# Performance work log

Measured on AMD Instinct MI355X. Metric: run time of the kernel, lower is better.

Reference implementation:

```python
import jax, jax.numpy as jnp
import numpy as np

B, T, H, F, K, NB, MAXL = 32, 512, 512, 512, 3, 256, 2048


def _conv1d(x, w, b, pad):
    # x: [B,T,Cin], w: [K,Cin,Cout] -> [B,T,Cout]
    y = jax.lax.conv_general_dilated(x, w, window_strides=(1,), padding=[(pad, pad)],
                                     dimension_numbers=('NWC', 'WIO', 'NWC'))
    return y + b


def _layernorm(x, g, b):
    m = jnp.mean(x, axis=-1, keepdims=True)
    v = jnp.mean((x - m) ** 2, axis=-1, keepdims=True)
    return (x - m) * jax.lax.rsqrt(v + 1e-5) * g + b


def _variance_predictor(x, mask, cw1, cb1, g1, b1, cw2, cb2, g2, b2, lw, lb, k):
    # ConvNorm(k, pad=(k-1)//2) -> ReLU -> LN -> ConvNorm(k, pad=1) -> ReLU -> LN -> Linear(F,1)
    h = _layernorm(jax.nn.relu(_conv1d(x, cw1, cb1, (k - 1) // 2)), g1, b1)
    h = _layernorm(jax.nn.relu(_conv1d(h, cw2, cb2, 1)), g2, b2)
    out = h @ lw + lb  # [B,T]
    return jnp.where(mask, 0.0, out)


def setup_inputs() -> dict:
    key = jax.random.key(0)
    ks = jax.random.split(key, 12)
    s = 0.02
    inp = {
        'x': jax.random.normal(ks[0], (B, T, H), jnp.float32),
        'src_mask': jnp.zeros((B, T), jnp.bool_),
        'duration': jax.random.randint(ks[1], (B, T), 0, 8),
        'pitch_target': jax.random.normal(ks[2], (B, T), jnp.float32),
        'energy_target': jax.random.normal(ks[3], (B, T), jnp.float32),
        # stacked predictor params: index 0=duration, 1=pitch, 2=energy
        'conv1_w': jax.random.normal(ks[4], (3, K, H, F), jnp.float32) * s,
        'conv1_b': jnp.zeros((3, F), jnp.float32),
        'ln1_g': jnp.ones((3, F), jnp.float32),
        'ln1_b': jnp.zeros((3, F), jnp.float32),
        'conv2_w': jax.random.normal(ks[5], (3, K, F, F), jnp.float32) * s,
        'conv2_b': jnp.zeros((3, F), jnp.float32),
        'ln2_g': jnp.ones((3, F), jnp.float32),
        'ln2_b': jnp.zeros((3, F), jnp.float32),
        'lin_w': jax.random.normal(ks[6], (3, F), jnp.float32) * s,
        'lin_b': jnp.zeros((3,), jnp.float32),
        'pitch_bins': jnp.linspace(-3.0, 3.0, NB - 1, dtype=jnp.float32),
        'energy_bins': jnp.linspace(-3.0, 3.0, NB - 1, dtype=jnp.float32),
        'pitch_table': jax.random.normal(ks[7], (NB, H), jnp.float32) * s,
        'energy_table': jax.random.normal(ks[8], (NB, H), jnp.float32) * s,
        'max_len': MAXL,
    }
    return inp


def reference(x, src_mask, duration, pitch_target, energy_target,
              conv1_w, conv1_b, ln1_g, ln1_b, conv2_w, conv2_b, ln2_g, ln2_b,
              lin_w, lin_b, pitch_bins, energy_bins, pitch_table, energy_table, max_len):
    k = conv1_w.shape[1]

    def vp(i, inp):
        return _variance_predictor(inp, src_mask, conv1_w[i], conv1_b[i], ln1_g[i], ln1_b[i],
                                   conv2_w[i], conv2_b[i], ln2_g[i], ln2_b[i], lin_w[i], lin_b[i], k)

    log_duration_pred = vp(0, x)
    # pitch: predict, bucketize target, add embedding (training path with targets)
    pitch_pred = vp(1, x)
    p_idx = jnp.searchsorted(pitch_bins, pitch_target)  # torch.bucketize
    x = x + pitch_table[p_idx]
    # energy on pitch-conditioned features
    energy_pred = vp(2, x)
    e_idx = jnp.searchsorted(energy_bins, energy_target)
    x = x + energy_table[e_idx]

    # LengthRegulator: expand each phoneme vec duration[b,i] times, pad to max_len
    dur = jnp.where(src_mask, 0, duration)
    cum = jnp.cumsum(dur, axis=1)                 # [B,T]
    mel_len = jnp.minimum(cum[:, -1], max_len)    # [B]
    frames = jnp.arange(max_len)
    idx = jax.vmap(lambda c: jnp.searchsorted(c, frames, side='right'))(cum)
    idx = jnp.clip(idx, 0, x.shape[1] - 1)        # [B,max_len]
    x_out = jnp.take_along_axis(x, idx[:, :, None], axis=1)  # [B,max_len,H]
    mel_mask = frames[None, :] >= mel_len[:, None]
    x_out = jnp.where(mel_mask[:, :, None], 0.0, x_out)
    return x_out, log_duration_pred, pitch_pred, energy_pred, mel_len, mel_mask
```

## Files before the change

### kernel.cpp

```cpp
#include <hip/hip_runtime.h>
#include <hip/hip_bf16.h>

typedef unsigned short ushort_t;
typedef unsigned int uint_t;
typedef __attribute__((ext_vector_type(8))) short bf16x8;
typedef __attribute__((ext_vector_type(4))) float f32x4;

#define NB_T 512
#define NB_B 32
#define NB_M (NB_B * NB_T)
#define KDIM 1536
#define MAXL 2048
#define EPI_STRIDE 144

__device__ __forceinline__ ushort_t f2bf(float f) {
  __hip_bfloat16 h = __float2bfloat16(f);
  return *reinterpret_cast<ushort_t*>(&h);
}
__device__ __forceinline__ float bf2f(ushort_t u) {
  __hip_bfloat16 h;
  *reinterpret_cast<ushort_t*>(&h) = u;
  return __bfloat162float(h);
}
__device__ __forceinline__ uint_t pack2(float a, float b) {
  return (uint_t)f2bf(a) | ((uint_t)f2bf(b) << 16);
}
__device__ __forceinline__ void gload_lds16(const void* g, void* l) {
  __builtin_amdgcn_global_load_lds((const __attribute__((address_space(1))) void*)g,
                                   (__attribute__((address_space(3))) void*)l, 16, 0, 0);
}

__global__ __launch_bounds__(256) void k_wt(const float* __restrict__ w, ushort_t* __restrict__ wt) {
  __shared__ float tile[64][65];
  const int pk = blockIdx.y;
  const int p = pk / 3, kk = pk % 3;
  const int ot = (blockIdx.x & 7) * 64;
  const int it = (blockIdx.x >> 3) * 64;
  const int tx = threadIdx.x & 63;
  const int ty = threadIdx.x >> 6;
  const float* src = w + (size_t)pk * 512 * 512;
  #pragma unroll
  for (int r = ty; r < 64; r += 4)
    tile[r][tx] = src[(size_t)(it + r) * 512 + ot + tx];
  __syncthreads();
  #pragma unroll
  for (int r = ty; r < 64; r += 4)
    wt[((size_t)(p * 512 + ot + r)) * KDIM + kk * 512 + it + tx] = f2bf(tile[tx][r]);
}

__global__ __launch_bounds__(256) void k_bucket(const float* __restrict__ pt, const float* __restrict__ et,
                                                const float* __restrict__ pb, const float* __restrict__ eb,
                                                int* __restrict__ pi, int* __restrict__ ei) {
  const int i = blockIdx.x * 256 + threadIdx.x;
  if (i >= NB_M) return;
  float v = pt[i];
  int lo = 0, hi = 255;
  while (lo < hi) { int mid = (lo + hi) >> 1; if (pb[mid] < v) lo = mid + 1; else hi = mid; }
  pi[i] = lo;
  v = et[i]; lo = 0; hi = 255;
  while (lo < hi) { int mid = (lo + hi) >> 1; if (eb[mid] < v) lo = mid + 1; else hi = mid; }
  ei[i] = lo;
}

__global__ __launch_bounds__(512) void k_cum(const int* __restrict__ dur, const unsigned char* __restrict__ mask,
                                             int* __restrict__ cum, float* __restrict__ mel_len_out,
                                             float* __restrict__ mel_mask_out) {
  __shared__ int s[512];
  const int b = blockIdx.x, t = threadIdx.x;
  int d = mask[b * NB_T + t] ? 0 : dur[b * NB_T + t];
  s[t] = d;
  __syncthreads();
  for (int off = 1; off < 512; off <<= 1) {
    int v = (t >= off) ? s[t - off] : 0;
    __syncthreads();
    s[t] += v;
    __syncthreads();
  }
  cum[b * NB_T + t] = s[t];
  int ml = s[511]; ml = ml < MAXL ? ml : MAXL;
  if (t == 0) mel_len_out[b] = (float)ml;
  for (int f = t; f < MAXL; f += 512)
    mel_mask_out[b * MAXL + f] = (f >= ml) ? 1.0f : 0.0f;
}

__global__ __launch_bounds__(256) void k_prep(const float* __restrict__ x,
                                              const float* __restrict__ ptab, const float* __restrict__ etab,
                                              const int* __restrict__ pidx, const int* __restrict__ eidx,
                                              ushort_t* __restrict__ xb_pad, ushort_t* __restrict__ x2pad,
                                              ushort_t* __restrict__ lnp2, float* __restrict__ x3f) {
  const int rp = blockIdx.x;
  const int b = rp / 514, j = rp % 514;
  const int tid = threadIdx.x;
  if (j == 0 || j == 513) {
    ((uint_t*)(xb_pad + (size_t)rp * 512))[tid] = 0u;
    ((uint_t*)(x2pad + (size_t)rp * 512))[tid] = 0u;
    ((uint_t*)(lnp2 + (size_t)rp * 512))[tid] = 0u;
    return;
  }
  const int m = b * NB_T + j - 1;
  const float2 xv = ((const float2*)(x + (size_t)m * 512))[tid];
  const float2 pv = ((const float2*)(ptab + (size_t)pidx[m] * 512))[tid];
  const float2 ev = ((const float2*)(etab + (size_t)eidx[m] * 512))[tid];
  ((uint_t*)(xb_pad + (size_t)rp * 512))[tid] = pack2(xv.x, xv.y);
  const float ax = xv.x + pv.x, ay = xv.y + pv.y;
  ((uint_t*)(x2pad + (size_t)rp * 512))[tid] = pack2(ax, ay);
  float2 o; o.x = ax + ev.x; o.y = ay + ev.y;
  ((float2*)(x3f + (size_t)m * 512))[tid] = o;
}

__global__ __launch_bounds__(256) void k_gemm(const ushort_t* __restrict__ A0,
                                              const ushort_t* __restrict__ A1,
                                              const ushort_t* __restrict__ A2,
                                              const ushort_t* __restrict__ Wt,
                                              const float* __restrict__ bias,
                                              ushort_t* __restrict__ H) {
  __shared__ short smem[18432];
  const int tid = threadIdx.x;
  const int lane = tid & 63, wid = tid >> 6;

  const int h = blockIdx.x;
  const int logical = (h & 7) * 192 + (h >> 3);
  const int pred = logical >> 9;
  const int tile = logical & 511;
  const int mt = tile >> 2, nt = tile & 3;
  const int m0 = mt * 128, n0 = nt * 128;
  const int b = m0 >> 9, t0 = m0 & 511;
  const long Arow0 = (long)b * 514 + t0 + 1;

  const ushort_t* Ap = (pred == 0) ? A0 : ((pred == 1) ? A1 : A2);
  const ushort_t* Wp = Wt + (size_t)pred * 512 * KDIM;
  const float* bp = bias + pred * 512;
  ushort_t* Hp = H + (size_t)pred * NB_M * 512;

  const int subr = lane >> 2;
  const int ioff = (lane & 3) * 8;
  const int wr = wid >> 1, wc = wid & 1;
  const int lr = lane & 15, kg = lane >> 4;

  f32x4 acc[4][4];
  #pragma unroll
  for (int i = 0; i < 4; ++i)
    #pragma unroll
    for (int j = 0; j < 4; ++j) acc[i][j] = (f32x4)0.f;

  auto STAGE = [&](int kk, int buf) {
    const int dt = (kk >> 4) - 1;
    const int i0 = (kk & 15) << 5;
    short* la = &smem[buf * 8192];
    short* lb = &smem[buf * 8192 + 4096];
    #pragma unroll
    for (int q = 0; q < 2; ++q) {
      const int chunk = wid * 2 + q;
      const int r = chunk * 16 + subr;
      gload_lds16(Ap + (size_t)(Arow0 + r + dt) * 512 + i0 + ioff, &la[chunk * 512]);
      gload_lds16(Wp + (size_t)(n0 + r) * KDIM + kk * 32 + ioff, &lb[chunk * 512]);
    }
  };

  STAGE(0, 0);
  __syncthreads();
  int buf = 0;
  for (int kk = 0; kk < 48; ++kk) {
    if (kk < 47) STAGE(kk + 1, buf ^ 1);
    const short* la = &smem[buf * 8192];
    const short* lb = &smem[buf * 8192 + 4096];
    bf16x8 af[4], bfv[4];
    #pragma unroll
    for (int fi = 0; fi < 4; ++fi)
      af[fi] = *(const bf16x8*)&la[(wr * 64 + fi * 16 + lr) * 32 + kg * 8];
    #pragma unroll
    for (int fj = 0; fj < 4; ++fj)
      bfv[fj] = *(const bf16x8*)&lb[(wc * 64 + fj * 16 + lr) * 32 + kg * 8];
    #pragma unroll
    for (int fi = 0; fi < 4; ++fi)
      #pragma unroll
      for (int fj = 0; fj < 4; ++fj)
        acc[fi][fj] = __builtin_amdgcn_mfma_f32_16x16x32_bf16(af[fi], bfv[fj], acc[fi][fj], 0, 0, 0);
    __syncthreads();
    buf ^= 1;
  }

  float bvv[4];
  #pragma unroll
  for (int fj = 0; fj < 4; ++fj) bvv[fj] = bp[n0 + wc * 64 + fj * 16 + lr];
  #pragma unroll
  for (int fi = 0; fi < 4; ++fi) {
    const int rowb = wr * 64 + fi * 16 + kg * 4;
    #pragma unroll
    for (int fj = 0; fj < 4; ++fj) {
      const int col = wc * 64 + fj * 16 + lr;
      #pragma unroll
      for (int r = 0; r < 4; ++r) {
        float v = acc[fi][fj][r] + bvv[fj];
        v = v > 0.f ? v : 0.f;
        smem[(rowb + r) * EPI_STRIDE + col] = (short)f2bf(v);
      }
    }
  }
  __syncthreads();
  #pragma unroll
  for (int s = 0; s < 8; ++s) {
    const int chunk = tid + s * 256;
    const int row = chunk >> 4, c8 = (chunk & 15) * 8;
    bf16x8 vv = *(const bf16x8*)&smem[row * EPI_STRIDE + c8];
    *(bf16x8*)(Hp + (size_t)(m0 + row) * 512 + n0 + c8) = vv;
  }
}

__global__ __launch_bounds__(256) void k_ln_mid(const ushort_t* __restrict__ Hh,
                                                const float* __restrict__ g, const float* __restrict__ bb,
                                                ushort_t* __restrict__ lnp0, ushort_t* __restrict__ lnp1,
                                                ushort_t* __restrict__ lnp2) {
  const int rr = blockIdx.x * 4 + (threadIdx.x >> 6);
  const int pred = rr >> 14, m = rr & (NB_M - 1);
  const int lane = threadIdx.x & 63;
  const float* gp = g + pred * 512;
  const float* bp = bb + pred * 512;
  ushort_t* dst = (pred == 0) ? lnp0 : ((pred == 1) ? lnp1 : lnp2);
  bf16x8 v = *(const bf16x8*)(Hh + (size_t)rr * 512 + lane * 8);
  float xv[8];
  float s = 0.f;
  #pragma unroll
  for (int j = 0; j < 8; ++j) { xv[j] = bf2f((ushort_t)v[j]); s += xv[j]; }
  #pragma unroll
  for (int mm = 32; mm >= 1; mm >>= 1) s += __shfl_xor(s, mm, 64);
  const float mean = s * (1.f / 512.f);
  float vs = 0.f;
  #pragma unroll
  for (int j = 0; j < 8; ++j) { float d = xv[j] - mean; vs += d * d; }
  #pragma unroll
  for (int mm = 32; mm >= 1; mm >>= 1) vs += __shfl_xor(vs, mm, 64);
  const float rstd = rsqrtf(vs * (1.f / 512.f) + 1e-5f);
  const float4 g0 = ((const float4*)(gp + lane * 8))[0];
  const float4 g1 = ((const float4*)(gp + lane * 8))[1];
  const float4 b0 = ((const float4*)(bp + lane * 8))[0];
  const float4 b1 = ((const float4*)(bp + lane * 8))[1];
  const float gg[8] = {g0.x, g0.y, g0.z, g0.w, g1.x, g1.y, g1.z, g1.w};
  const float bv[8] = {b0.x, b0.y, b0.z, b0.w, b1.x, b1.y, b1.z, b1.w};
  bf16x8 o;
  #pragma unroll
  for (int j = 0; j < 8; ++j) o[j] = (short)f2bf((xv[j] - mean) * rstd * gg[j] + bv[j]);
  const int bidx = m >> 9, t = m & 511;
  *(bf16x8*)(dst + ((size_t)(bidx * 514 + t + 1)) * 512 + lane * 8) = o;
}

__global__ __launch_bounds__(256) void k_ln_fin(const ushort_t* __restrict__ Hh,
                                                const float* __restrict__ g, const float* __restrict__ bb,
                                                const float* __restrict__ lw, const float* __restrict__ lbp,
                                                const unsigned char* __restrict__ mask,
                                                float* __restrict__ outp) {
  const int rr = blockIdx.x * 4 + (threadIdx.x >> 6);
  const int pred = rr >> 14, m = rr & (NB_M - 1);
  const int lane = threadIdx.x & 63;
  const float* gp = g + pred * 512;
  const float* bp = bb + pred * 512;
  const float* wp = lw + pred * 512;
  bf16x8 v = *(const bf16x8*)(Hh + (size_t)rr * 512 + lane * 8);
  float xv[8];
  float s = 0.f;
  #pragma unroll
  for (int j = 0; j < 8; ++j) { xv[j] = bf2f((ushort_t)v[j]); s += xv[j]; }
  #pragma unroll
  for (int mm = 32; mm >= 1; mm >>= 1) s += __shfl_xor(s, mm, 64);
  const float mean = s * (1.f / 512.f);
  float vs = 0.f;
  #pragma unroll
  for (int j = 0; j < 8; ++j) { float d = xv[j] - mean; vs += d * d; }
  #pragma unroll
  for (int mm = 32; mm >= 1; mm >>= 1) vs += __shfl_xor(vs, mm, 64);
  const float rstd = rsqrtf(vs * (1.f / 512.f) + 1e-5f);
  const float4 g0 = ((const float4*)(gp + lane * 8))[0];
  const float4 g1 = ((const float4*)(gp + lane * 8))[1];
  const float4 b0 = ((const float4*)(bp + lane * 8))[0];
  const float4 b1 = ((const float4*)(bp + lane * 8))[1];
  const float4 w0 = ((const float4*)(wp + lane * 8))[0];
  const float4 w1 = ((const float4*)(wp + lane * 8))[1];
  const float gg[8] = {g0.x, g0.y, g0.z, g0.w, g1.x, g1.y, g1.z, g1.w};
  const float bv[8] = {b0.x, b0.y, b0.z, b0.w, b1.x, b1.y, b1.z, b1.w};
  const float ww[8] = {w0.x, w0.y, w0.z, w0.w, w1.x, w1.y, w1.z, w1.w};
  float dot = 0.f;
  #pragma unroll
  for (int j = 0; j < 8; ++j) dot += ((xv[j] - mean) * rstd * gg[j] + bv[j]) * ww[j];
  #pragma unroll
  for (int mm = 32; mm >= 1; mm >>= 1) dot += __shfl_xor(dot, mm, 64);
  if (lane == 0) {
    float val = dot + lbp[pred];
    if (mask[m]) val = 0.f;
    outp[pred * NB_M + m] = val;
  }
}

__global__ __launch_bounds__(128) void k_regulate(const float* __restrict__ x3f, const int* __restrict__ cum,
                                                  float* __restrict__ xout) {
  const int bid = blockIdx.x;
  const int b = bid >> 11, f = bid & 2047;
  const int* c = cum + b * NB_T;
  int ml = c[511]; ml = ml < MAXL ? ml : MAXL;
  const int tid = threadIdx.x;
  float4 val = make_float4(0.f, 0.f, 0.f, 0.f);
  if (f < ml) {
    int lo = 0, hi = 512;
    while (lo < hi) { int mid = (lo + hi) >> 1; if (c[mid] <= f) lo = mid + 1; else hi = mid; }
    if (lo > 511) lo = 511;
    val = ((const float4*)(x3f + ((size_t)(b * NB_T + lo)) * 512))[tid];
  }
  ((float4*)(xout + ((size_t)(b * MAXL + f)) * 512))[tid] = val;
}

extern "C" void kernel_launch(void* const* d_in, const int* in_sizes, int n_in,
                              void* d_out, int out_size, void* d_ws, size_t ws_size,
                              hipStream_t stream) {
  const float* x        = (const float*)d_in[0];
  const unsigned char* src_mask = (const unsigned char*)d_in[1];
  const int* duration   = (const int*)d_in[2];
  const float* pitch_t  = (const float*)d_in[3];
  const float* energy_t = (const float*)d_in[4];
  const float* conv1_w  = (const float*)d_in[5];
  const float* conv1_b  = (const float*)d_in[6];
  const float* ln1_g    = (const float*)d_in[7];
  const float* ln1_b    = (const float*)d_in[8];
  const float* conv2_w  = (const float*)d_in[9];
  const float* conv2_b  = (const float*)d_in[10];
  const float* ln2_g    = (const float*)d_in[11];
  const float* ln2_b    = (const float*)d_in[12];
  const float* lin_w    = (const float*)d_in[13];
  const float* lin_b    = (const float*)d_in[14];
  const float* pbins    = (const float*)d_in[15];
  const float* ebins    = (const float*)d_in[16];
  const float* ptab     = (const float*)d_in[17];
  const float* etab     = (const float*)d_in[18];

  char* ws = (char*)d_ws;
  ushort_t* wt1    = (ushort_t*)(ws + 0);
  ushort_t* wt2    = (ushort_t*)(ws + 4718592);
  ushort_t* xb_pad = (ushort_t*)(ws + 9437184);
  ushort_t* x2pad  = (ushort_t*)(ws + 26279936);
  ushort_t* lnp2   = (ushort_t*)(ws + 43122688);
  ushort_t* hbuf   = (ushort_t*)(ws + 59965440);
  float*    x3f    = (float*)   (ws + 110297088);
  int*      p_idx  = (int*)     (ws + 143851520);
  int*      e_idx  = (int*)     (ws + 143917056);
  int*      cum    = (int*)     (ws + 143982592);

  float* out      = (float*)d_out;
  float* o_xout   = out;
  float* o_preds  = out + 33554432;
  float* o_mellen = o_preds + 3 * NB_M;
  float* o_mmask  = o_mellen + 32;

  k_bucket<<<NB_M / 256, 256, 0, stream>>>(pitch_t, energy_t, pbins, ebins, p_idx, e_idx);
  k_cum<<<NB_B, 512, 0, stream>>>(duration, src_mask, cum, o_mellen, o_mmask);
  k_wt<<<dim3(64, 9), 256, 0, stream>>>(conv1_w, wt1);
  k_wt<<<dim3(64, 9), 256, 0, stream>>>(conv2_w, wt2);
  k_prep<<<NB_B * 514, 256, 0, stream>>>(x, ptab, etab, p_idx, e_idx, xb_pad, x2pad, lnp2, x3f);

  k_gemm<<<1536, 256, 0, stream>>>(xb_pad, xb_pad, x2pad, wt1, conv1_b, hbuf);
  k_ln_mid<<<3 * NB_M / 4, 256, 0, stream>>>(hbuf, ln1_g, ln1_b, xb_pad, x2pad, lnp2);
  k_gemm<<<1536, 256, 0, stream>>>(xb_pad, x2pad, lnp2, wt2, conv2_b, hbuf);
  k_ln_fin<<<3 * NB_M / 4, 256, 0, stream>>>(hbuf, ln2_g, ln2_b, lin_w, lin_b, src_mask, o_preds);

  k_regulate<<<NB_B * MAXL, 128, 0, stream>>>(x3f, cum, o_xout);
}
```

Before: 503.2 us.

## Fuse bucketize into prep, merge weight transposes, store x3 in bf16, restructure regulate

The bucketize binary search moves into k_prep, which removes a kernel launch and the p_idx/e_idx round trip. The two weight-transpose launches become a single launch. The pitch- and energy-conditioned features are stored as bf16 instead of fp32, halving that intermediate write and the regulator's gather reads. k_regulate is rewritten so each block caches the cumsum in LDS, handles 64 frames and also writes mel_mask, which lets k_cum drop that write; the cost is bf16 rounding on the x_out output values.

```diff
diff --git a/kernel.cpp b/kernel.cpp
--- a/kernel.cpp
+++ b/kernel.cpp
@@ -30,41 +30,30 @@
                                    (__attribute__((address_space(3))) void*)l, 16, 0, 0);
 }
 
-__global__ __launch_bounds__(256) void k_wt(const float* __restrict__ w, ushort_t* __restrict__ wt) {
+__global__ __launch_bounds__(256) void k_wt(const float* __restrict__ w1, const float* __restrict__ w2,
+                                            ushort_t* __restrict__ wt1, ushort_t* __restrict__ wt2) {
   __shared__ float tile[64][65];
-  const int pk = blockIdx.y;
-  const int p = pk / 3, kk = pk % 3;
+  int g = blockIdx.y;
+  const float* wsrc;
+  ushort_t* wdst;
+  if (g < 9) { wsrc = w1; wdst = wt1; } else { wsrc = w2; wdst = wt2; g -= 9; }
+  const int p = g / 3, kk = g % 3;
   const int ot = (blockIdx.x & 7) * 64;
   const int it = (blockIdx.x >> 3) * 64;
   const int tx = threadIdx.x & 63;
   const int ty = threadIdx.x >> 6;
-  const float* src = w + (size_t)pk * 512 * 512;
+  const float* src = wsrc + (size_t)g * 512 * 512;
   #pragma unroll
   for (int r = ty; r < 64; r += 4)
     tile[r][tx] = src[(size_t)(it + r) * 512 + ot + tx];
   __syncthreads();
   #pragma unroll
   for (int r = ty; r < 64; r += 4)
-    wt[((size_t)(p * 512 + ot + r)) * KDIM + kk * 512 + it + tx] = f2bf(tile[tx][r]);
-}
-
-__global__ __launch_bounds__(256) void k_bucket(const float* __restrict__ pt, const float* __restrict__ et,
-                                                const float* __restrict__ pb, const float* __restrict__ eb,
-                                                int* __restrict__ pi, int* __restrict__ ei) {
-  const int i = blockIdx.x * 256 + threadIdx.x;
-  if (i >= NB_M) return;
-  float v = pt[i];
-  int lo = 0, hi = 255;
-  while (lo < hi) { int mid = (lo + hi) >> 1; if (pb[mid] < v) lo = mid + 1; else hi = mid; }
-  pi[i] = lo;
-  v = et[i]; lo = 0; hi = 255;
-  while (lo < hi) { int mid = (lo + hi) >> 1; if (eb[mid] < v) lo = mid + 1; else hi = mid; }
-  ei[i] = lo;
+    wdst[((size_t)(p * 512 + ot + r)) * KDIM + kk * 512 + it + tx] = f2bf(tile[tx][r]);
 }
 
 __global__ __launch_bounds__(512) void k_cum(const int* __restrict__ dur, const unsigned char* __restrict__ mask,
-                                             int* __restrict__ cum, float* __restrict__ mel_len_out,
-                                             float* __restrict__ mel_mask_out) {
+                                             int* __restrict__ cum, float* __restrict__ mel_len_out) {
   __shared__ int s[512];
   const int b = blockIdx.x, t = threadIdx.x;
   int d = mask[b * NB_T + t] ? 0 : dur[b * NB_T + t];
@@ -77,17 +66,18 @@
     __syncthreads();
   }
   cum[b * NB_T + t] = s[t];
-  int ml = s[511]; ml = ml < MAXL ? ml : MAXL;
-  if (t == 0) mel_len_out[b] = (float)ml;
-  for (int f = t; f < MAXL; f += 512)
-    mel_mask_out[b * MAXL + f] = (f >= ml) ? 1.0f : 0.0f;
+  if (t == 0) {
+    int ml = s[511]; ml = ml < MAXL ? ml : MAXL;
+    mel_len_out[b] = (float)ml;
+  }
 }
 
 __global__ __launch_bounds__(256) void k_prep(const float* __restrict__ x,
+                                              const float* __restrict__ pt, const float* __restrict__ et,
+                                              const float* __restrict__ pb, const float* __restrict__ eb,
                                               const float* __restrict__ ptab, const float* __restrict__ etab,
-                                              const int* __restrict__ pidx, const int* __restrict__ eidx,
                                               ushort_t* __restrict__ xb_pad, ushort_t* __restrict__ x2pad,
-                                              ushort_t* __restrict__ lnp2, float* __restrict__ x3f) {
+                                              ushort_t* __restrict__ lnp2, ushort_t* __restrict__ x3b) {
   const int rp = blockIdx.x;
   const int b = rp / 514, j = rp % 514;
   const int tid = threadIdx.x;
@@ -98,14 +88,21 @@
     return;
   }
   const int m = b * NB_T + j - 1;
+  float v = pt[m];
+  int lo = 0, hi = 255;
+  while (lo < hi) { int mid = (lo + hi) >> 1; if (pb[mid] < v) lo = mid + 1; else hi = mid; }
+  const int pi = lo;
+  v = et[m]; lo = 0; hi = 255;
+  while (lo < hi) { int mid = (lo + hi) >> 1; if (eb[mid] < v) lo = mid + 1; else hi = mid; }
+  const int ei = lo;
+
   const float2 xv = ((const float2*)(x + (size_t)m * 512))[tid];
-  const float2 pv = ((const float2*)(ptab + (size_t)pidx[m] * 512))[tid];
-  const float2 ev = ((const float2*)(etab + (size_t)eidx[m] * 512))[tid];
+  const float2 pv = ((const float2*)(ptab + (size_t)pi * 512))[tid];
+  const float2 ev = ((const float2*)(etab + (size_t)ei * 512))[tid];
   ((uint_t*)(xb_pad + (size_t)rp * 512))[tid] = pack2(xv.x, xv.y);
   const float ax = xv.x + pv.x, ay = xv.y + pv.y;
   ((uint_t*)(x2pad + (size_t)rp * 512))[tid] = pack2(ax, ay);
-  float2 o; o.x = ax + ev.x; o.y = ay + ev.y;
-  ((float2*)(x3f + (size_t)m * 512))[tid] = o;
+  ((uint_t*)(x3b + (size_t)m * 512))[tid] = pack2(ax + ev.x, ay + ev.y);
 }
 
 __global__ __launch_bounds__(256) void k_gemm(const ushort_t* __restrict__ A0,
@@ -290,21 +287,33 @@
   }
 }
 
-__global__ __launch_bounds__(128) void k_regulate(const float* __restrict__ x3f, const int* __restrict__ cum,
-                                                  float* __restrict__ xout) {
-  const int bid = blockIdx.x;
-  const int b = bid >> 11, f = bid & 2047;
-  const int* c = cum + b * NB_T;
+__global__ __launch_bounds__(256) void k_regulate(const ushort_t* __restrict__ x3b, const int* __restrict__ cum,
+                                                  float* __restrict__ xout, float* __restrict__ mmask) {
+  __shared__ int c[512];
+  const int blk = blockIdx.x;
+  const int b = blk >> 5, chunk = blk & 31;
+  const int tid = threadIdx.x, lane = tid & 63, w = tid >> 6;
+  c[tid] = cum[b * NB_T + tid];
+  c[tid + 256] = cum[b * NB_T + tid + 256];
+  __syncthreads();
   int ml = c[511]; ml = ml < MAXL ? ml : MAXL;
-  const int tid = threadIdx.x;
-  float4 val = make_float4(0.f, 0.f, 0.f, 0.f);
-  if (f < ml) {
-    int lo = 0, hi = 512;
-    while (lo < hi) { int mid = (lo + hi) >> 1; if (c[mid] <= f) lo = mid + 1; else hi = mid; }
-    if (lo > 511) lo = 511;
-    val = ((const float4*)(x3f + ((size_t)(b * NB_T + lo)) * 512))[tid];
-  }
-  ((float4*)(xout + ((size_t)(b * MAXL + f)) * 512))[tid] = val;
+  const int f0 = chunk * 64 + w * 16;
+  for (int i = 0; i < 16; ++i) {
+    const int f = f0 + i;
+    float o[8] = {0.f, 0.f, 0.f, 0.f, 0.f, 0.f, 0.f, 0.f};
+    if (f < ml) {
+      int lo = 0, hi = 512;
+      while (lo < hi) { int mid = (lo + hi) >> 1; if (c[mid] <= f) lo = mid + 1; else hi = mid; }
+      if (lo > 511) lo = 511;
+      bf16x8 vv = *(const bf16x8*)(x3b + ((size_t)(b * NB_T + lo)) * 512 + lane * 8);
+      #pragma unroll
+      for (int j = 0; j < 8; ++j) o[j] = bf2f((ushort_t)vv[j]);
+    }
+    float* dst = xout + ((size_t)(b * MAXL + f)) * 512 + lane * 8;
+    ((float4*)dst)[0] = make_float4(o[0], o[1], o[2], o[3]);
+    ((float4*)dst)[1] = make_float4(o[4], o[5], o[6], o[7]);
+    if (lane == 0) mmask[b * MAXL + f] = (f >= ml) ? 1.0f : 0.0f;
+  }
 }
 
 extern "C" void kernel_launch(void* const* d_in, const int* in_sizes, int n_in,
@@ -337,10 +346,8 @@
   ushort_t* x2pad  = (ushort_t*)(ws + 26279936);
   ushort_t* lnp2   = (ushort_t*)(ws + 43122688);
   ushort_t* hbuf   = (ushort_t*)(ws + 59965440);
-  float*    x3f    = (float*)   (ws + 110297088);
-  int*      p_idx  = (int*)     (ws + 143851520);
-  int*      e_idx  = (int*)     (ws + 143917056);
-  int*      cum    = (int*)     (ws + 143982592);
+  ushort_t* x3b    = (ushort_t*)(ws + 110297088);
+  int*      cum    = (int*)     (ws + 127074304);
 
   float* out      = (float*)d_out;
   float* o_xout   = out;
@@ -348,16 +355,15 @@
   float* o_mellen = o_preds + 3 * NB_M;
   float* o_mmask  = o_mellen + 32;
 
-  k_bucket<<<NB_M / 256, 256, 0, stream>>>(pitch_t, energy_t, pbins, ebins, p_idx, e_idx);
-  k_cum<<<NB_B, 512, 0, stream>>>(duration, src_mask, cum, o_mellen, o_mmask);
-  k_wt<<<dim3(64, 9), 256, 0, stream>>>(conv1_w, wt1);
-  k_wt<<<dim3(64, 9), 256, 0, stream>>>(conv2_w, wt2);
-  k_prep<<<NB_B * 514, 256, 0, stream>>>(x, ptab, etab, p_idx, e_idx, xb_pad, x2pad, lnp2, x3f);
+  k_cum<<<NB_B, 512, 0, stream>>>(duration, src_mask, cum, o_mellen);
+  k_wt<<<dim3(64, 18), 256, 0, stream>>>(conv1_w, conv2_w, wt1, wt2);
+  k_prep<<<NB_B * 514, 256, 0, stream>>>(x, pitch_t, energy_t, pbins, ebins, ptab, etab,
+                                         xb_pad, x2pad, lnp2, x3b);
 
   k_gemm<<<1536, 256, 0, stream>>>(xb_pad, xb_pad, x2pad, wt1, conv1_b, hbuf);
   k_ln_mid<<<3 * NB_M / 4, 256, 0, stream>>>(hbuf, ln1_g, ln1_b, xb_pad, x2pad, lnp2);
   k_gemm<<<1536, 256, 0, stream>>>(xb_pad, x2pad, lnp2, wt2, conv2_b, hbuf);
   k_ln_fin<<<3 * NB_M / 4, 256, 0, stream>>>(hbuf, ln2_g, ln2_b, lin_w, lin_b, src_mask, o_preds);
 
-  k_regulate<<<NB_B * MAXL, 128, 0, stream>>>(x3f, cum, o_xout);
-}
+  k_regulate<<<1024, 256, 0, stream>>>(x3b, cum, o_xout, o_mmask);
+}
```

New measurement: 496.0 us. About the same (-1.4%).
